# Kernel tuning notes

Measured on AMD Instinct MI355X. Metric: run time of the kernel, lower is better.

## Reference

```python
import jax, jax.numpy as jnp
import numpy as np

B_MOL = 512      # molecules in batch
A_PER = 64       # atoms per molecule (uniform -> scopes are regular)
EU_PER = 2 * A_PER   # undirected bonds per molecule (ring + skip ring)
ED_PER = 2 * EU_PER  # directed bonds per molecule
N_ATOMS = B_MOL * A_PER
N_DIR = B_MOL * ED_PER
AF, BF = 98, 111
H, HEADS, DEPTH, MLP = 256, 8, 10, 512
DK = H // HEADS
ATOM_OUT, BOND_OUT = 128, 32


def _graph_indices():
    ar = np.arange(A_PER)
    su = np.concatenate([ar, ar])
    du = np.concatenate([(ar + 1) % A_PER, (ar + 2) % A_PER])
    src = np.concatenate([su, du])   # directed: fwd then rev copies
    dst = np.concatenate([du, su])
    rev = np.concatenate([np.arange(EU_PER) + EU_PER, np.arange(EU_PER)])
    offa = (np.arange(B_MOL) * A_PER)[:, None]
    offb = (np.arange(B_MOL) * ED_PER)[:, None]
    b2a = (src[None] + offa).reshape(-1).astype(np.int32)
    b2t = (dst[None] + offa).reshape(-1).astype(np.int32)
    b2rev = (rev[None] + offb).reshape(-1).astype(np.int32)
    pairs = np.stack([(su[None] + offa).reshape(-1), (du[None] + offa).reshape(-1)], 1).astype(np.int32)
    return jnp.asarray(b2a), jnp.asarray(b2t), jnp.asarray(b2rev), jnp.asarray(pairs)


def setup_inputs() -> dict:
    key = jax.random.key(0)
    ks = jax.random.split(key, 24)
    g = lambda k, s: jax.random.normal(k, s, jnp.float32) / np.sqrt(s[0])
    b2a, b2t, b2rev, bond_pairs = _graph_indices()
    return {
        'f_atoms': jax.random.normal(ks[0], (N_ATOMS, AF), jnp.float32),
        'f_bonds': jax.random.normal(ks[1], (N_DIR, BF), jnp.float32),
        'prev_hid': jnp.zeros((N_ATOMS, H), jnp.float32),
        'b2a': b2a, 'b2t': b2t, 'b2rev': b2rev, 'bond_pairs': bond_pairs,
        'W_i': g(ks[2], (BF, H)), 'W_h': g(ks[3], (H, H)),
        'W_o': g(ks[4], (AF + H, H)), 'b_o': jnp.zeros((H,), jnp.float32),
        'Wq': g(ks[5], (H, H)), 'Wk': g(ks[6], (H, H)),
        'Wv': g(ks[7], (H, H)), 'Wattn': g(ks[8], (H, H)),
        'W_vv': jnp.eye(H, dtype=jnp.float32), 'W_vc': g(ks[9], (H, H)),
        'A1': g(ks[10], (H, MLP)), 'a1': jnp.zeros((MLP,), jnp.float32),
        'A2': g(ks[11], (MLP, ATOM_OUT)), 'a2': jnp.zeros((ATOM_OUT,), jnp.float32),
        'B1': g(ks[12], (2 * H, MLP)), 'b1': jnp.zeros((MLP,), jnp.float32),
        'B2': g(ks[13], (MLP, BOND_OUT)), 'b2b': jnp.zeros((BOND_OUT,), jnp.float32),
        'G1': g(ks[14], (H, MLP)), 'g1': jnp.zeros((MLP,), jnp.float32),
        'G2': g(ks[15], (MLP, 1)), 'g2': jnp.zeros((1,), jnp.float32),
    }


def reference(f_atoms, f_bonds, prev_hid, b2a, b2t, b2rev, bond_pairs,
              W_i, W_h, W_o, b_o, Wq, Wk, Wv, Wattn, W_vv, W_vc,
              A1, a1, A2, a2, B1, b1, B2, b2b, G1, g1, G2, g2):
    # ---- DMPNN encoder (directed bond messages) ----
    h0 = jax.nn.relu(f_bonds @ W_i)                     # [E_dir, H]
    h = h0
    for _ in range(DEPTH - 1):
        a_sum = jax.ops.segment_sum(h, b2t, num_segments=N_ATOMS)  # incoming msg per atom
        m = a_sum[b2a] - h[b2rev]                       # exclude reverse bond
        h = jax.nn.relu(h0 + m @ W_h)
    a_in = jax.ops.segment_sum(h, b2t, num_segments=N_ATOMS)
    a_feats = jax.nn.relu(jnp.concatenate([f_atoms, a_in], 1) @ W_o + b_o)  # [N, H]

    # ---- Global_Attention over per-molecule scopes (uniform sizes -> reshape) ----
    x = a_feats.reshape(B_MOL, A_PER, H)
    q = (x @ Wq).reshape(B_MOL, A_PER, HEADS, DK)
    k = (x @ Wk).reshape(B_MOL, A_PER, HEADS, DK)
    v = (x @ Wv).reshape(B_MOL, A_PER, HEADS, DK)
    scores = jnp.einsum('bqhd,bkhd->bhqk', q, k) / np.sqrt(DK)
    attn = jax.nn.softmax(scores, axis=-1)
    ctx = jnp.einsum('bhqk,bkhd->bqhd', attn, v).reshape(B_MOL, A_PER, H)
    a_feats = (x + ctx @ Wattn).reshape(N_ATOMS, H)     # residual MHA

    # ---- recurrent atom state update ----
    atom_feats = jax.nn.relu(prev_hid @ W_vv.T + a_feats @ W_vc.T)  # [N, H]

    # ---- gather-based readout heads ----
    bond_feats = jnp.concatenate([atom_feats[bond_pairs[:, 0]],
                                  atom_feats[bond_pairs[:, 1]]], axis=1)  # [E_und, 2H]
    graph_vecs = atom_feats.reshape(B_MOL, A_PER, H).sum(axis=1)          # [B, H]

    atom_outs = jax.nn.relu(atom_feats @ A1 + a1) @ A2 + a2   # [N, ATOM_OUT]
    bond_outs = jax.nn.relu(bond_feats @ B1 + b1) @ B2 + b2b  # [E_und, BOND_OUT]
    graph_outs = jax.nn.relu(graph_vecs @ G1 + g1) @ G2 + g2  # [B, 1]

    # per-molecule edit scores: [bond scores | atom scores | graph score]
    edit_scores = jnp.concatenate([bond_outs.reshape(B_MOL, -1),
                                   atom_outs.reshape(B_MOL, -1),
                                   graph_outs], axis=1)
    return edit_scores
```

## Files before the change

kernel.cpp:

```cpp
#include <hip/hip_runtime.h>
#include <cstdint>
#include <cstddef>

#define B_MOL 512
#define A_PER 64
#define ED_PER 256
#define N_ATOMS (B_MOL * A_PER)
#define N_DIR (B_MOL * ED_PER)
#define N_UND (B_MOL * 128)
#define HID 256
#define OUT_STRIDE 12289
#define AP 40
#define CP 72

typedef __attribute__((ext_vector_type(8))) short bf16x8;
typedef __attribute__((ext_vector_type(8))) unsigned short u16x8;
typedef __attribute__((ext_vector_type(4))) float f32x4;

#define MFMA(a, b, c) __builtin_amdgcn_mfma_f32_16x16x32_bf16(a, b, c, 0, 0, 0)

__device__ __forceinline__ float b2f(unsigned short s) {
  return __builtin_bit_cast(float, (unsigned)s << 16);
}
__device__ __forceinline__ void split2(float v, unsigned short& h, unsigned short& l) {
  unsigned ub = __builtin_bit_cast(unsigned, v);
  h = (unsigned short)(ub >> 16);
  float fh = __builtin_bit_cast(float, ub & 0xffff0000u);
  float r = v - fh;
  l = (unsigned short)(__builtin_bit_cast(unsigned, r) >> 16);
}
__device__ __forceinline__ unsigned short f2bf_rne(float v) {
  unsigned u = __builtin_bit_cast(unsigned, v);
  u += 0x7FFFu + ((u >> 16) & 1u);
  return (unsigned short)(u >> 16);
}
__device__ __forceinline__ int e_src(int e) {
  return (e < 64) ? e : (e < 128) ? (e - 64)
       : (e < 192) ? ((e - 127) & 63) : ((e - 190) & 63);
}

__global__ __launch_bounds__(256) void convAll(
    const float* Wi, const float* Wh, const float* Wo,
    const float* Wq, const float* Wk, const float* Wv,
    const float* Wattn, const float* Wvc, const float* Wvv,
    const float* A1, const float* A2, const float* B1, const float* B2,
    const float* fbF, unsigned short* fbT,
    unsigned short* WiTh, unsigned short* WiTl,
    unsigned short* WhTh, unsigned short* WhTl,
    unsigned short* WoTh, unsigned short* WoTl,
    unsigned short* WqkvTh, unsigned short* WqkvTl,
    unsigned short* WaTh, unsigned short* WaTl,
    unsigned short* Wcv2Th, unsigned short* Wcv2Tl,
    unsigned short* A1Th, unsigned short* A1Tl,
    unsigned short* A2Th, unsigned short* A2Tl,
    unsigned short* B1bTh, unsigned short* B1bTl,
    unsigned short* B2Th, unsigned short* B2Tl) {
  int b = blockIdx.x;
  if (b >= 3744) {
    int e = (b - 3744) * 32 + (threadIdx.x >> 3);
    int ks = (threadIdx.x & 7) * 16;
    const float* s = fbF + (size_t)e * 111;
    u16x8 o0 = {0,0,0,0,0,0,0,0}, o1 = {0,0,0,0,0,0,0,0};
#pragma unroll
    for (int z = 0; z < 8; ++z) {
      int k = ks + z;
      if (k < 111) o0[z] = f2bf_rne(s[k]);
    }
#pragma unroll
    for (int z = 0; z < 8; ++z) {
      int k = ks + 8 + z;
      if (k < 111) o1[z] = f2bf_rne(s[k]);
    }
    *(u16x8*)&fbT[(size_t)e * 128 + ks] = o0;
    *(u16x8*)&fbT[(size_t)e * 128 + ks + 8] = o1;
    return;
  }
  if (b >= 1792 && b < 2048) {
    int n = b & 255;
    for (int k = threadIdx.x; k < 768; k += 256) {
      float v;
      if (k < 256) {
        v = 0.f;
        for (int j = 0; j < 256; ++j)
          v += Wattn[(size_t)k * 256 + j] * Wvc[(size_t)n * 256 + j];
      } else if (k < 512) {
        v = Wvc[(size_t)n * 256 + (k - 256)];
      } else {
        v = Wvv[(size_t)n * 256 + (k - 512)];
      }
      unsigned short h_, l_;
      split2(v, h_, l_);
      Wcv2Th[(size_t)n * 768 + k] = h_;
      Wcv2Tl[(size_t)n * 768 + k] = l_;
    }
    return;
  }
  if (b >= 2688 && b < 3712) {
    int n = b - 2688;
    int k = threadIdx.x;
    float v = (n < 512) ? B1[(size_t)k * 512 + n]
                        : B1[(size_t)(k + 256) * 512 + (n - 512)];
    unsigned short h_, l_;
    split2(v, h_, l_);
    B1bTh[(size_t)n * 256 + k] = h_;
    B1bTl[(size_t)n * 256 + k] = l_;
    return;
  }
  const float* src = nullptr;
  unsigned short *dh = nullptr, *dl = nullptr;
  int K = 256, N = 256, Kp = 256, n = 0;
  if (b < 1792) {
    int seg = b >> 8; n = b & 255;
    switch (seg) {
      case 0: src = Wi; dh = WiTh; dl = WiTl; K = 111; Kp = 128; break;
      case 1: src = Wh; dh = WhTh; dl = WhTl; break;
      case 2: src = Wo; dh = WoTh; dl = WoTl; K = 354; Kp = 384; break;
      case 3: src = Wq; dh = WqkvTh; dl = WqkvTl; break;
      case 4: src = Wk; dh = WqkvTh + 65536; dl = WqkvTl + 65536; break;
      case 5: src = Wv; dh = WqkvTh + 131072; dl = WqkvTl + 131072; break;
      default: src = Wattn; dh = WaTh; dl = WaTl; break;
    }
    for (int k = threadIdx.x; k < Kp; k += 256) {
      float v = 0.f;
      if (b >> 8 == 2) {
        if (k < 256) v = src[(size_t)(98 + k) * 256 + n];
        else if (k < 354) v = src[(size_t)(k - 256) * 256 + n];
      } else {
        if (k < K) v = src[(size_t)k * N + n];
      }
      unsigned short h_, l_;
      split2(v, h_, l_);
      dh[(size_t)n * Kp + k] = h_;
      dl[(size_t)n * Kp + k] = l_;
    }
    return;
  }
  if (b < 2560)      { n = b - 2048; src = A1; dh = A1Th; dl = A1Tl; K = 256; N = 512; Kp = 256; }
  else if (b < 2688) { n = b - 2560; src = A2; dh = A2Th; dl = A2Tl; K = 512; N = 128; Kp = 512; }
  else               { n = b - 3712; src = B2; dh = B2Th; dl = B2Tl; K = 512; N = 32;  Kp = 512; }
  for (int k = threadIdx.x; k < Kp; k += 256) {
    float v = (k < K) ? src[(size_t)k * N + n] : 0.f;
    unsigned short h_, l_;
    split2(v, h_, l_);
    dh[(size_t)n * Kp + k] = h_;
    dl[(size_t)n * Kp + k] = l_;
  }
}

template <int AMODE>
__launch_bounds__(256, 3)
__global__ void mgemm(const void* Aa_, const void* Ab_, const void* Ac_, const void* Ad_,
                      const float* __restrict__ Af32,
                      const unsigned short* __restrict__ BTh,
                      const unsigned short* __restrict__ BTl, int ldb,
                      const unsigned short* addH, const unsigned short* addL,
                      const float* __restrict__ bias,
                      const float* __restrict__ abias,
                      void* outA, void* outB,
                      int M, int N, int K, int lda, int ldco, int outcol,
                      int relu, int outmode) {
  __shared__ unsigned short AsH[128 * AP], AsL[128 * AP];
  __shared__ unsigned short BsH[128 * AP], BsL[128 * AP];
  const int tid = threadIdx.x;
  const int lane = tid & 63;
  const int l15 = lane & 15, l4 = lane >> 4;
  const int w = tid >> 6;
  const int wr = (w >> 1) * 64, wc = (w & 1) * 64;
  const int tileM = blockIdx.x * 128, tileN = blockIdx.y * 128;
  const int srow = tid >> 1;
  const int sks = (tid & 1) * 16;

  int rem = N - tileN - wc;
  int bnMax = rem >= 64 ? 4 : (rem > 0 ? (rem >> 4) : 0);

  f32x4 zf = {0.f, 0.f, 0.f, 0.f};
  f32x4 acc[4][4];
#pragma unroll
  for (int i = 0; i < 4; ++i)
#pragma unroll
    for (int j = 0; j < 4; ++j) acc[i][j] = zf;

  const int nkb = (K + 31) >> 5;
  for (int kb = 0; kb < nkb; ++kb) {
    __syncthreads();
    const int k0 = kb * 32 + sks;
    {
      const int row = tileM + srow;
      if (AMODE == 6) {
        const unsigned short* Ah = (const unsigned short*)Aa_;
        size_t bse = (size_t)row * lda + k0;
        *(u16x8*)&AsH[srow * AP + sks]     = *(const u16x8*)&Ah[bse];
        *(u16x8*)&AsH[srow * AP + sks + 8] = *(const u16x8*)&Ah[bse + 8];
      } else if (AMODE == 1 || (AMODE == 7 && k0 < 512)) {
        const unsigned short* Ah; const unsigned short* Al;
        size_t bse;
        if (AMODE == 7) {
          Ah = (k0 < 256) ? (const unsigned short*)Aa_ : (const unsigned short*)Ac_;
          Al = (k0 < 256) ? (const unsigned short*)Ab_ : (const unsigned short*)Ad_;
          bse = (size_t)row * 256 + (k0 & 255);
        } else {
          Ah = (const unsigned short*)Aa_;
          Al = (const unsigned short*)Ab_;
          bse = (size_t)row * lda + k0;
        }
        *(u16x8*)&AsH[srow * AP + sks]     = *(const u16x8*)&Ah[bse];
        *(u16x8*)&AsH[srow * AP + sks + 8] = *(const u16x8*)&Ah[bse + 8];
        *(u16x8*)&AsL[srow * AP + sks]     = *(const u16x8*)&Al[bse];
        *(u16x8*)&AsL[srow * AP + sks + 8] = *(const u16x8*)&Al[bse + 8];
      } else if (AMODE == 5) {
        int mol = row >> 7, u = row & 127;
        int a0 = (u < 64) ? u : (u - 64);
        int a1v = (u < 64) ? ((u + 1) & 63) : ((u - 62) & 63);
        size_t p1 = (size_t)(mol * 64 + a0) * 1024 + k0;
        size_t p2 = (size_t)(mol * 64 + a1v) * 1024 + 512 + k0;
        const unsigned short* Ph = (const unsigned short*)Aa_;
        const unsigned short* Pl = (const unsigned short*)Ab_;
        u16x8 x1h[2] = {*(const u16x8*)&Ph[p1], *(const u16x8*)&Ph[p1 + 8]};
        u16x8 x1l[2] = {*(const u16x8*)&Pl[p1], *(const u16x8*)&Pl[p1 + 8]};
        u16x8 x2h[2] = {*(const u16x8*)&Ph[p2], *(const u16x8*)&Ph[p2 + 8]};
        u16x8 x2l[2] = {*(const u16x8*)&Pl[p2], *(const u16x8*)&Pl[p2 + 8]};
#pragma unroll
        for (int c = 0; c < 2; ++c) {
          u16x8 hv, lv;
#pragma unroll
          for (int z = 0; z < 8; ++z) {
            float v = b2f(x1h[c][z]) + b2f(x1l[c][z])
                    + b2f(x2h[c][z]) + b2f(x2l[c][z]) + abias[k0 + c * 8 + z];
            v = fmaxf(v, 0.f);
            unsigned short h_, l_;
            split2(v, h_, l_);
            hv[z] = h_; lv[z] = l_;
          }
          *(u16x8*)&AsH[srow * AP + sks + c * 8] = hv;
          *(u16x8*)&AsL[srow * AP + sks + c * 8] = lv;
        }
      } else if (AMODE == 8 && k0 < 256) {
        int mol = row >> 6, t = row & 63;
        const float* hb = Af32 + (size_t)mol * 65536;
        int ea0 = (t + 63) & 63;
        int ea1 = 64 + ((t + 62) & 63);
        int ea2 = 128 + t;
        int ea3 = 192 + t;
#pragma unroll
        for (int half = 0; half < 2; ++half) {
          int kk = k0 + half * 8;
          f32x4 s0, s1;
          {
            const float* p = hb + (size_t)ea0 * 256 + kk;
            s0 = *(const f32x4*)p;
            s1 = *(const f32x4*)(p + 4);
          }
          {
            const float* p = hb + (size_t)ea1 * 256 + kk;
            s0 += *(const f32x4*)p;
            s1 += *(const f32x4*)(p + 4);
          }
          {
            const float* p = hb + (size_t)ea2 * 256 + kk;
            s0 += *(const f32x4*)p;
            s1 += *(const f32x4*)(p + 4);
          }
          {
            const float* p = hb + (size_t)ea3 * 256 + kk;
            s0 += *(const f32x4*)p;
            s1 += *(const f32x4*)(p + 4);
          }
          u16x8 hv, lv;
#pragma unroll
          for (int z = 0; z < 4; ++z) {
            unsigned short h_, l_;
            split2(s0[z], h_, l_); hv[z] = h_; lv[z] = l_;
            split2(s1[z], h_, l_); hv[4 + z] = h_; lv[4 + z] = l_;
          }
          *(u16x8*)&AsH[srow * AP + sks + half * 8] = hv;
          *(u16x8*)&AsL[srow * AP + sks + half * 8] = lv;
        }
      } else {
        u16x8 hv0 = {0,0,0,0,0,0,0,0}, lv0 = {0,0,0,0,0,0,0,0};
        u16x8 hv1 = {0,0,0,0,0,0,0,0}, lv1 = {0,0,0,0,0,0,0,0};
#pragma unroll
        for (int z = 0; z < 16; ++z) {
          int k = k0 + z;
          float v = 0.f;
          if (AMODE == 0) {
            if (k < K) v = ((const float*)Aa_)[(size_t)row * lda + k];
          } else if (AMODE == 2) {
            if (k < 256) v = ((const float*)Aa_)[(size_t)row * 256 + k];
            else if (k < 354) v = ((const float*)Ab_)[(size_t)row * 98 + (k - 256)];
          } else if (AMODE == 8) {
            if (k < 354) v = ((const float*)Ab_)[(size_t)row * 98 + (k - 256)];
          } else {
            v = Af32[(size_t)row * 256 + (k - 512)];
          }
          unsigned short h_, l_;
          split2(v, h_, l_);
          if (z < 8) { hv0[z] = h_; lv0[z] = l_; }
          else       { hv1[z - 8] = h_; lv1[z - 8] = l_; }
        }
        *(u16x8*)&AsH[srow * AP + sks]     = hv0;
        *(u16x8*)&AsH[srow * AP + sks + 8] = hv1;
        *(u16x8*)&AsL[srow * AP + sks]     = lv0;
        *(u16x8*)&AsL[srow * AP + sks + 8] = lv1;
      }
    }
    {
      const int n = tileN + srow;
      if (n < N) {
        size_t bb = (size_t)n * ldb + k0;
        *(u16x8*)&BsH[srow * AP + sks]     = *(const u16x8*)&BTh[bb];
        *(u16x8*)&BsH[srow * AP + sks + 8] = *(const u16x8*)&BTh[bb + 8];
        *(u16x8*)&BsL[srow * AP + sks]     = *(const u16x8*)&BTl[bb];
        *(u16x8*)&BsL[srow * AP + sks + 8] = *(const u16x8*)&BTl[bb + 8];
      } else {
        u16x8 z8 = {0,0,0,0,0,0,0,0};
        *(u16x8*)&BsH[srow * AP + sks]     = z8;
        *(u16x8*)&BsH[srow * AP + sks + 8] = z8;
        *(u16x8*)&BsL[srow * AP + sks]     = z8;
        *(u16x8*)&BsL[srow * AP + sks + 8] = z8;
      }
    }
    __syncthreads();
    bf16x8 ah[4], al[4];
#pragma unroll
    for (int am = 0; am < 4; ++am) {
      int ar = wr + am * 16 + l15;
      ah[am] = *(const bf16x8*)&AsH[ar * AP + l4 * 8];
      if (AMODE != 6) al[am] = *(const bf16x8*)&AsL[ar * AP + l4 * 8];
    }
#pragma unroll
    for (int bn = 0; bn < 4; ++bn) {
      if (bn < bnMax) {
        int br = wc + bn * 16 + l15;
        bf16x8 bh = *(const bf16x8*)&BsH[br * AP + l4 * 8];
        bf16x8 bl = *(const bf16x8*)&BsL[br * AP + l4 * 8];
#pragma unroll
        for (int am = 0; am < 4; ++am) {
          acc[am][bn] = MFMA(ah[am], bh, acc[am][bn]);
          acc[am][bn] = MFMA(ah[am], bl, acc[am][bn]);
          if (AMODE != 6) acc[am][bn] = MFMA(al[am], bh, acc[am][bn]);
        }
      }
    }
  }

#pragma unroll
  for (int am = 0; am < 4; ++am) {
#pragma unroll
    for (int bn = 0; bn < 4; ++bn) {
      if (bn >= bnMax) continue;
      int col = tileN + wc + bn * 16 + l15;
      float bs = bias ? bias[col] : 0.f;
#pragma unroll
      for (int r = 0; r < 4; ++r) {
        size_t row = (size_t)tileM + wr + am * 16 + l4 * 4 + r;
        float v = acc[am][bn][r] + bs;
        if (addH) v += b2f(addH[row * 256 + col]) + b2f(addL[row * 256 + col]);
        if (relu) v = fmaxf(v, 0.f);
        if (outmode == 0) {
          unsigned short h_, l_;
          split2(v, h_, l_);
          ((unsigned short*)outA)[row * (size_t)ldco + col] = h_;
          ((unsigned short*)outB)[row * (size_t)ldco + col] = l_;
        } else if (outmode == 1) {
          ((float*)outA)[row * (size_t)ldco + outcol + col] = v;
        } else if (outmode == 2) {
          int mol = (int)(row >> 6), t = (int)(row & 63);
          ((float*)outA)[(size_t)mol * OUT_STRIDE + 4096 + t * 128 + col] = v;
        } else {
          int mol = (int)(row >> 7), u = (int)(row & 127);
          ((float*)outA)[(size_t)mol * OUT_STRIDE + u * 32 + col] = v;
        }
      }
    }
  }
}

__launch_bounds__(1024)
__global__ void msg_f4(float* h,
                       const unsigned short* __restrict__ WhTh,
                       const unsigned short* __restrict__ WhTl,
                       const unsigned short* __restrict__ WiTh,
                       const unsigned short* __restrict__ WiTl,
                       const unsigned short* __restrict__ fbT) {
  extern __shared__ char smem_[];
  unsigned short* AsC = (unsigned short*)smem_;
  unsigned short* BsC = (unsigned short*)(smem_ + 36864);
  const int tid = threadIdx.x;
  const int lane = tid & 63, l15 = lane & 15, l4 = lane >> 4;
  const int w = tid >> 6;
  const int wm = (w >> 2) * 64;
  const int wn = (w & 3) * 64;
  const int mol = blockIdx.x;
  const int arow = tid >> 2;
  const int aks = (tid & 3) * 8;

  f32x4 acc[4][4];
#pragma unroll
  for (int i = 0; i < 4; ++i)
#pragma unroll
    for (int j = 0; j < 4; ++j) acc[i][j] = (f32x4){0.f, 0.f, 0.f, 0.f};

  const int sA = e_src(arow);
  const int rvA = (arow < 128) ? (arow + 128) : (arow - 128);
  const int i0 = (sA + 63) & 63;
  const int i1 = 64 + ((sA + 62) & 63);
  const int i2 = 128 + sA;
  const int i3 = 192 + sA;
  const size_t hbase = (size_t)mol * 256 * 256;

  const size_t fbb = (size_t)(mol * 256 + arow) * 128;
  for (int kb = 0; kb < 4; ++kb) {
    __syncthreads();
    {
      *(u16x8*)&AsC[arow * CP + aks] = *(const u16x8*)&fbT[fbb + kb * 32 + aks];
    }
    {
      size_t bb = (size_t)arow * 128 + kb * 32 + aks;
      *(u16x8*)&BsC[arow * CP + aks]      = *(const u16x8*)&WiTh[bb];
      *(u16x8*)&BsC[arow * CP + 32 + aks] = *(const u16x8*)&WiTl[bb];
    }
    __syncthreads();
    bf16x8 ah[4];
#pragma unroll
    for (int am = 0; am < 4; ++am) {
      int ar = wm + am * 16 + l15;
      ah[am] = *(const bf16x8*)&AsC[ar * CP + l4 * 8];
    }
#pragma unroll
    for (int bn = 0; bn < 4; ++bn) {
      int br = wn + bn * 16 + l15;
      bf16x8 bh = *(const bf16x8*)&BsC[br * CP + l4 * 8];
      bf16x8 bl = *(const bf16x8*)&BsC[br * CP + 32 + l4 * 8];
#pragma unroll
      for (int am = 0; am < 4; ++am) {
        acc[am][bn] = MFMA(ah[am], bh, acc[am][bn]);
        acc[am][bn] = MFMA(ah[am], bl, acc[am][bn]);
      }
    }
  }
#pragma unroll
  for (int i = 0; i < 4; ++i)
#pragma unroll
    for (int j = 0; j < 4; ++j)
#pragma unroll
      for (int r = 0; r < 4; ++r) acc[i][j][r] = fmaxf(acc[i][j][r], 0.f);

  for (int kb = 0; kb < 8; ++kb) {
    __syncthreads();
    {
      const int c0 = kb * 32 + aks;
      f32x4 m0, m1;
      {
        const float* p = &h[hbase + (size_t)i0 * 256 + c0];
        m0 = *(const f32x4*)p;
        m1 = *(const f32x4*)(p + 4);
      }
      {
        const float* p = &h[hbase + (size_t)i1 * 256 + c0];
        m0 += *(const f32x4*)p;
        m1 += *(const f32x4*)(p + 4);
      }
      {
        const float* p = &h[hbase + (size_t)i2 * 256 + c0];
        m0 += *(const f32x4*)p;
        m1 += *(const f32x4*)(p + 4);
      }
      {
        const float* p = &h[hbase + (size_t)i3 * 256 + c0];
        m0 += *(const f32x4*)p;
        m1 += *(const f32x4*)(p + 4);
      }
      {
        const float* p = &h[hbase + (size_t)rvA * 256 + c0];
        m0 -= *(const f32x4*)p;
        m1 -= *(const f32x4*)(p + 4);
      }
      u16x8 hv, lv;
#pragma unroll
      for (int z = 0; z < 4; ++z) {
        unsigned short h_, l_;
        split2(m0[z], h_, l_); hv[z] = h_; lv[z] = l_;
        split2(m1[z], h_, l_); hv[4 + z] = h_; lv[4 + z] = l_;
      }
      *(u16x8*)&AsC[arow * CP + aks]      = hv;
      *(u16x8*)&AsC[arow * CP + 32 + aks] = lv;
    }
    {
      size_t bb = (size_t)arow * 256 + kb * 32 + aks;
      *(u16x8*)&BsC[arow * CP + aks]      = *(const u16x8*)&WhTh[bb];
      *(u16x8*)&BsC[arow * CP + 32 + aks] = *(const u16x8*)&WhTl[bb];
    }
    __syncthreads();
    bf16x8 ah[4], al[4];
#pragma unroll
    for (int am = 0; am < 4; ++am) {
      int ar = wm + am * 16 + l15;
      ah[am] = *(const bf16x8*)&AsC[ar * CP + l4 * 8];
      al[am] = *(const bf16x8*)&AsC[ar * CP + 32 + l4 * 8];
    }
#pragma unroll
    for (int bn = 0; bn < 4; ++bn) {
      int br = wn + bn * 16 + l15;
      bf16x8 bh = *(const bf16x8*)&BsC[br * CP + l4 * 8];
      bf16x8 bl = *(const bf16x8*)&BsC[br * CP + 32 + l4 * 8];
#pragma unroll
      for (int am = 0; am < 4; ++am) {
        acc[am][bn] = MFMA(ah[am], bh, acc[am][bn]);
        acc[am][bn] = MFMA(ah[am], bl, acc[am][bn]);
        acc[am][bn] = MFMA(al[am], bh, acc[am][bn]);
      }
    }
  }

#pragma unroll
  for (int am = 0; am < 4; ++am) {
#pragma unroll
    for (int r = 0; r < 4; ++r) {
      int row = wm + am * 16 + l4 * 4 + r;
      size_t rowb = hbase + (size_t)row * 256;
#pragma unroll
      for (int bn = 0; bn < 4; ++bn) {
        int col = wn + bn * 16 + l15;
        h[rowb + col] = fmaxf(acc[am][bn][r], 0.f);
      }
    }
  }
}

__global__ __launch_bounds__(64) void attn_k(const float* __restrict__ qkv,
                                             unsigned short* __restrict__ ctxH,
                                             unsigned short* __restrict__ ctxL) {
  __shared__ float kls[64 * 32];
  __shared__ float vls[64 * 32];
  int mol = blockIdx.x >> 3, head = blockIdx.x & 7;
  int lane = threadIdx.x;
  size_t rb = ((size_t)(mol * 64 + lane)) * 768 + head * 32;
#pragma unroll
  for (int c = 0; c < 8; ++c) {
    *(float4*)(kls + lane * 32 + c * 4) = *(const float4*)(qkv + rb + 256 + c * 4);
    *(float4*)(vls + lane * 32 + c * 4) = *(const float4*)(qkv + rb + 512 + c * 4);
  }
  float q[32];
#pragma unroll
  for (int d = 0; d < 32; ++d) q[d] = qkv[rb + d];
  __syncthreads();
  float mx = -1e30f, l = 0.f;
  float acc[32];
#pragma unroll
  for (int d = 0; d < 32; ++d) acc[d] = 0.f;
  for (int j = 0; j < 64; ++j) {
    float s = 0.f;
#pragma unroll
    for (int d = 0; d < 32; ++d) s += q[d] * kls[j * 32 + d];
    s *= 0.17677669529663687f;
    float nm = fmaxf(mx, s);
    float co = __expf(mx - nm);
    float p = __expf(s - nm);
    l = l * co + p;
#pragma unroll
    for (int d = 0; d < 32; ++d) acc[d] = acc[d] * co + p * vls[j * 32 + d];
    mx = nm;
  }
  float inv = 1.f / l;
  size_t ob = ((size_t)(mol * 64 + lane)) * 256 + head * 32;
#pragma unroll
  for (int d = 0; d < 32; ++d) {
    unsigned short h_, l_;
    split2(acc[d] * inv, h_, l_);
    ctxH[ob + d] = h_;
    ctxL[ob + d] = l_;
  }
}

__global__ __launch_bounds__(512) void gvh_k(const unsigned short* __restrict__ afH,
                                             const unsigned short* __restrict__ afL,
                                             const float* __restrict__ G1,
                                             const float* __restrict__ g1,
                                             const float* __restrict__ G2,
                                             const float* __restrict__ g2,
                                             float* __restrict__ out) {
  __shared__ float xs[256];
  __shared__ float red[512];
  int mol = blockIdx.x, j = threadIdx.x;
  if (j < 256) {
    float s = 0.f;
    for (int a = 0; a < 64; ++a) {
      size_t i = ((size_t)mol * 64 + a) * 256 + j;
      s += b2f(afH[i]) + b2f(afL[i]);
    }
    xs[j] = s;
  }
  __syncthreads();
  float s = 0.f;
  for (int k = 0; k < 256; ++k) s += xs[k] * G1[k * 512 + j];
  s = fmaxf(s + g1[j], 0.f);
  red[j] = s * G2[j];
  __syncthreads();
  for (int st = 256; st > 0; st >>= 1) {
    if (j < st) red[j] += red[j + st];
    __syncthreads();
  }
  if (j == 0) out[(size_t)mol * OUT_STRIDE + 12288] = red[0] + g2[0];
}

extern "C" void kernel_launch(void* const* d_in, const int* in_sizes, int n_in,
                              void* d_out, int out_size, void* d_ws, size_t ws_size,
                              hipStream_t stream) {
  (void)in_sizes; (void)n_in; (void)out_size; (void)ws_size;
  const float* f_atoms  = (const float*)d_in[0];
  const float* f_bonds  = (const float*)d_in[1];
  const float* prev_hid = (const float*)d_in[2];
  const float* W_i   = (const float*)d_in[7];
  const float* W_h   = (const float*)d_in[8];
  const float* W_o   = (const float*)d_in[9];
  const float* b_o   = (const float*)d_in[10];
  const float* Wq    = (const float*)d_in[11];
  const float* Wk    = (const float*)d_in[12];
  const float* Wv    = (const float*)d_in[13];
  const float* Wattn = (const float*)d_in[14];
  const float* W_vv  = (const float*)d_in[15];
  const float* W_vc  = (const float*)d_in[16];
  const float* A1    = (const float*)d_in[17];
  const float* a1    = (const float*)d_in[18];
  const float* A2    = (const float*)d_in[19];
  const float* a2    = (const float*)d_in[20];
  const float* B1    = (const float*)d_in[21];
  const float* b1    = (const float*)d_in[22];
  const float* B2    = (const float*)d_in[23];
  const float* b2b   = (const float*)d_in[24];
  const float* G1    = (const float*)d_in[25];
  const float* g1    = (const float*)d_in[26];
  const float* G2    = (const float*)d_in[27];
  const float* g2    = (const float*)d_in[28];
  float* out = (float*)d_out;

  char* base = (char*)d_ws;
  float* h = (float*)(base);
  unsigned short* fbT = (unsigned short*)(base + 134217728);
  char* W0 = base + 167772160;
  unsigned short* WiTh   = (unsigned short*)(W0);
  unsigned short* WiTl   = (unsigned short*)(W0 + 65536);
  unsigned short* WhTh   = (unsigned short*)(W0 + 131072);
  unsigned short* WhTl   = (unsigned short*)(W0 + 262144);
  unsigned short* WoTh   = (unsigned short*)(W0 + 393216);
  unsigned short* WoTl   = (unsigned short*)(W0 + 589824);
  unsigned short* WqkvTh = (unsigned short*)(W0 + 786432);
  unsigned short* WqkvTl = (unsigned short*)(W0 + 1179648);
  unsigned short* WaTh   = (unsigned short*)(W0 + 1572864);
  unsigned short* WaTl   = (unsigned short*)(W0 + 1703936);
  unsigned short* Wcv2Th = (unsigned short*)(W0 + 1835008);
  unsigned short* Wcv2Tl = (unsigned short*)(W0 + 2228224);
  unsigned short* A1Th   = (unsigned short*)(W0 + 2621440);
  unsigned short* A1Tl   = (unsigned short*)(W0 + 2883584);
  unsigned short* A2Th   = (unsigned short*)(W0 + 3145728);
  unsigned short* A2Tl   = (unsigned short*)(W0 + 3276800);
  unsigned short* B1bTh  = (unsigned short*)(W0 + 3407872);
  unsigned short* B1bTl  = (unsigned short*)(W0 + 3932160);
  unsigned short* B2Th   = (unsigned short*)(W0 + 4456448);
  unsigned short* B2Tl   = (unsigned short*)(W0 + 4489216);
  unsigned short* xAh  = (unsigned short*)(base + 134217728);
  unsigned short* xAl  = (unsigned short*)(base + 150994944);
  float* qkv           = (float*)(base + 33554432);
  unsigned short* ctxh = (unsigned short*)(base);
  unsigned short* ctxl = (unsigned short*)(base + 16777216);
  unsigned short* atfh = (unsigned short*)(base + 67108864);
  unsigned short* atfl = (unsigned short*)(base + 83886080);
  unsigned short* t1h  = (unsigned short*)(base);
  unsigned short* t1l  = (unsigned short*)(base + 33554432);
  unsigned short* Ph   = (unsigned short*)(base);
  unsigned short* Pl   = (unsigned short*)(base + 100663296);

  convAll<<<7840, 256, 0, stream>>>(
      W_i, W_h, W_o, Wq, Wk, Wv, Wattn, W_vc, W_vv, A1, A2, B1, B2,
      f_bonds, fbT,
      WiTh, WiTl, WhTh, WhTl, WoTh, WoTl, WqkvTh, WqkvTl, WaTh, WaTl,
      Wcv2Th, Wcv2Tl, A1Th, A1Tl, A2Th, A2Tl, B1bTh, B1bTl, B2Th, B2Tl);

  mgemm<6><<<dim3(1024, 2), 256, 0, stream>>>(
      fbT, nullptr, nullptr, nullptr, nullptr, WiTh, WiTl, 128,
      nullptr, nullptr, nullptr, nullptr,
      h, nullptr, N_DIR, 256, 128, 128, 256, 0, 1, 1);

  for (int d = 0; d < 9; ++d) {
    msg_f4<<<512, 1024, 73728, stream>>>(h, WhTh, WhTl, WiTh, WiTl, fbT);
  }

  mgemm<8><<<dim3(256, 2), 256, 0, stream>>>(
      nullptr, f_atoms, nullptr, nullptr, h, WoTh, WoTl, 384,
      nullptr, nullptr, b_o, nullptr,
      xAh, xAl, N_ATOMS, 256, 354, 0, 256, 0, 1, 0);
  mgemm<1><<<dim3(256, 6), 256, 0, stream>>>(
      xAh, xAl, nullptr, nullptr, nullptr, WqkvTh, WqkvTl, 256,
      nullptr, nullptr, nullptr, nullptr,
      qkv, nullptr, N_ATOMS, 768, 256, 256, 768, 0, 0, 1);
  attn_k<<<4096, 64, 0, stream>>>(qkv, ctxh, ctxl);
  mgemm<7><<<dim3(256, 2), 256, 0, stream>>>(
      ctxh, ctxl, xAh, xAl, prev_hid, Wcv2Th, Wcv2Tl, 768,
      nullptr, nullptr, nullptr, nullptr,
      atfh, atfl, N_ATOMS, 256, 768, 256, 256, 0, 1, 0);
  mgemm<1><<<dim3(256, 4), 256, 0, stream>>>(
      atfh, atfl, nullptr, nullptr, nullptr, A1Th, A1Tl, 256,
      nullptr, nullptr, a1, nullptr,
      t1h, t1l, N_ATOMS, 512, 256, 256, 512, 0, 1, 0);
  mgemm<1><<<dim3(256, 1), 256, 0, stream>>>(
      t1h, t1l, nullptr, nullptr, nullptr, A2Th, A2Tl, 512,
      nullptr, nullptr, a2, nullptr,
      out, nullptr, N_ATOMS, 128, 512, 512, 0, 0, 0, 2);
  mgemm<1><<<dim3(256, 8), 256, 0, stream>>>(
      atfh, atfl, nullptr, nullptr, nullptr, B1bTh, B1bTl, 256,
      nullptr, nullptr, nullptr, nullptr,
      Ph, Pl, N_ATOMS, 1024, 256, 256, 1024, 0, 0, 0);
  mgemm<5><<<dim3(512, 1), 256, 0, stream>>>(
      Ph, Pl, nullptr, nullptr, nullptr, B2Th, B2Tl, 512,
      nullptr, nullptr, b2b, b1,
      out, nullptr, N_UND, 32, 512, 0, 0, 0, 0, 3);
  gvh_k<<<512, 512, 0, stream>>>(atfh, atfl, G1, g1, G2, g2, out);
}
```

Baseline: 1.724 ms.

## Double-buffer LDS in fused message-passing kernel to overlap staging with MFMA

Turns the msg kernel's two separate K loops (the W_i input part and the W_h message part) into a single 12-chunk loop with two LDS buffers. Chunk c+1 is staged while chunk c is computed, so there is one barrier per chunk instead of two. LDS use doubles to 144KB per block. That fits the 160KB LDS on MI355X, but with 1024-thread blocks only one block fits per CU either way. The relu on the input part is applied after chunk 3. The reads of h for the next chunk now overlap with MFMA work, which may add register pressure.

```diff
diff --git a/kernel.cpp b/kernel.cpp
--- a/kernel.cpp
+++ b/kernel.cpp
@@ -12,6 +12,7 @@
 #define OUT_STRIDE 12289
 #define AP 40
 #define CP 72
+#define BUFB 73728
 
 typedef __attribute__((ext_vector_type(8))) short bf16x8;
 typedef __attribute__((ext_vector_type(8))) unsigned short u16x8;
@@ -376,15 +377,13 @@
 }
 
 __launch_bounds__(1024)
-__global__ void msg_f4(float* h,
+__global__ void msg_f6(float* h,
                        const unsigned short* __restrict__ WhTh,
                        const unsigned short* __restrict__ WhTl,
                        const unsigned short* __restrict__ WiTh,
                        const unsigned short* __restrict__ WiTl,
                        const unsigned short* __restrict__ fbT) {
   extern __shared__ char smem_[];
-  unsigned short* AsC = (unsigned short*)smem_;
-  unsigned short* BsC = (unsigned short*)(smem_ + 36864);
   const int tid = threadIdx.x;
   const int lane = tid & 63, l15 = lane & 15, l4 = lane >> 4;
   const int w = tid >> 6;
@@ -407,48 +406,18 @@
   const int i2 = 128 + sA;
   const int i3 = 192 + sA;
   const size_t hbase = (size_t)mol * 256 * 256;
-
   const size_t fbb = (size_t)(mol * 256 + arow) * 128;
-  for (int kb = 0; kb < 4; ++kb) {
-    __syncthreads();
-    {
-      *(u16x8*)&AsC[arow * CP + aks] = *(const u16x8*)&fbT[fbb + kb * 32 + aks];
-    }
-    {
-      size_t bb = (size_t)arow * 128 + kb * 32 + aks;
+
+  auto STAGE = [&](int b, int c) {
+    unsigned short* AsC = (unsigned short*)(smem_ + b * BUFB);
+    unsigned short* BsC = (unsigned short*)(smem_ + b * BUFB + 36864);
+    if (c < 4) {
+      *(u16x8*)&AsC[arow * CP + aks] = *(const u16x8*)&fbT[fbb + c * 32 + aks];
+      size_t bb = (size_t)arow * 128 + c * 32 + aks;
       *(u16x8*)&BsC[arow * CP + aks]      = *(const u16x8*)&WiTh[bb];
       *(u16x8*)&BsC[arow * CP + 32 + aks] = *(const u16x8*)&WiTl[bb];
-    }
-    __syncthreads();
-    bf16x8 ah[4];
-#pragma unroll
-    for (int am = 0; am < 4; ++am) {
-      int ar = wm + am * 16 + l15;
-      ah[am] = *(const bf16x8*)&AsC[ar * CP + l4 * 8];
-    }
-#pragma unroll
-    for (int bn = 0; bn < 4; ++bn) {
-      int br = wn + bn * 16 + l15;
-      bf16x8 bh = *(const bf16x8*)&BsC[br * CP + l4 * 8];
-      bf16x8 bl = *(const bf16x8*)&BsC[br * CP + 32 + l4 * 8];
-#pragma unroll
-      for (int am = 0; am < 4; ++am) {
-        acc[am][bn] = MFMA(ah[am], bh, acc[am][bn]);
-        acc[am][bn] = MFMA(ah[am], bl, acc[am][bn]);
-      }
-    }
-  }
-#pragma unroll
-  for (int i = 0; i < 4; ++i)
-#pragma unroll
-    for (int j = 0; j < 4; ++j)
-#pragma unroll
-      for (int r = 0; r < 4; ++r) acc[i][j][r] = fmaxf(acc[i][j][r], 0.f);
-
-  for (int kb = 0; kb < 8; ++kb) {
-    __syncthreads();
-    {
-      const int c0 = kb * 32 + aks;
+    } else {
+      const int c0 = (c - 4) * 32 + aks;
       f32x4 m0, m1;
       {
         const float* p = &h[hbase + (size_t)i0 * 256 + c0];
@@ -484,31 +453,68 @@
       }
       *(u16x8*)&AsC[arow * CP + aks]      = hv;
       *(u16x8*)&AsC[arow * CP + 32 + aks] = lv;
-    }
-    {
-      size_t bb = (size_t)arow * 256 + kb * 32 + aks;
+      size_t bb = (size_t)arow * 256 + (c - 4) * 32 + aks;
       *(u16x8*)&BsC[arow * CP + aks]      = *(const u16x8*)&WhTh[bb];
       *(u16x8*)&BsC[arow * CP + 32 + aks] = *(const u16x8*)&WhTl[bb];
     }
+  };
+
+  auto COMPUTE = [&](int b, int c) {
+    unsigned short* AsC = (unsigned short*)(smem_ + b * BUFB);
+    unsigned short* BsC = (unsigned short*)(smem_ + b * BUFB + 36864);
+    if (c < 4) {
+      bf16x8 ah[4];
+#pragma unroll
+      for (int am = 0; am < 4; ++am) {
+        int ar = wm + am * 16 + l15;
+        ah[am] = *(const bf16x8*)&AsC[ar * CP + l4 * 8];
+      }
+#pragma unroll
+      for (int bn = 0; bn < 4; ++bn) {
+        int br = wn + bn * 16 + l15;
+        bf16x8 bh = *(const bf16x8*)&BsC[br * CP + l4 * 8];
+        bf16x8 bl = *(const bf16x8*)&BsC[br * CP + 32 + l4 * 8];
+#pragma unroll
+        for (int am = 0; am < 4; ++am) {
+          acc[am][bn] = MFMA(ah[am], bh, acc[am][bn]);
+          acc[am][bn] = MFMA(ah[am], bl, acc[am][bn]);
+        }
+      }
+    } else {
+      bf16x8 ah[4], al[4];
+#pragma unroll
+      for (int am = 0; am < 4; ++am) {
+        int ar = wm + am * 16 + l15;
+        ah[am] = *(const bf16x8*)&AsC[ar * CP + l4 * 8];
+        al[am] = *(const bf16x8*)&AsC[ar * CP + 32 + l4 * 8];
+      }
+#pragma unroll
+      for (int bn = 0; bn < 4; ++bn) {
+        int br = wn + bn * 16 + l15;
+        bf16x8 bh = *(const bf16x8*)&BsC[br * CP + l4 * 8];
+        bf16x8 bl = *(const bf16x8*)&BsC[br * CP + 32 + l4 * 8];
+#pragma unroll
+        for (int am = 0; am < 4; ++am) {
+          acc[am][bn] = MFMA(ah[am], bh, acc[am][bn]);
+          acc[am][bn] = MFMA(ah[am], bl, acc[am][bn]);
+          acc[am][bn] = MFMA(al[am], bh, acc[am][bn]);
+        }
+      }
+    }
+  };
+
+  STAGE(0, 0);
+  for (int c = 0; c < 12; ++c) {
     __syncthreads();
-    bf16x8 ah[4], al[4];
-#pragma unroll
-    for (int am = 0; am < 4; ++am) {
-      int ar = wm + am * 16 + l15;
-      ah[am] = *(const bf16x8*)&AsC[ar * CP + l4 * 8];
-      al[am] = *(const bf16x8*)&AsC[ar * CP + 32 + l4 * 8];
-    }
-#pragma unroll
-    for (int bn = 0; bn < 4; ++bn) {
-      int br = wn + bn * 16 + l15;
-      bf16x8 bh = *(const bf16x8*)&BsC[br * CP + l4 * 8];
-      bf16x8 bl = *(const bf16x8*)&BsC[br * CP + 32 + l4 * 8];
-#pragma unroll
-      for (int am = 0; am < 4; ++am) {
-        acc[am][bn] = MFMA(ah[am], bh, acc[am][bn]);
-        acc[am][bn] = MFMA(ah[am], bl, acc[am][bn]);
-        acc[am][bn] = MFMA(al[am], bh, acc[am][bn]);
-      }
+    if (c + 1 < 12) STAGE((c + 1) & 1, c + 1);
+    COMPUTE(c & 1, c);
+    if (c == 3) {
+#pragma unroll
+      for (int i = 0; i < 4; ++i)
+#pragma unroll
+        for (int j = 0; j < 4; ++j)
+#pragma unroll
+          for (int r = 0; r < 4; ++r) acc[i][j][r] = fmaxf(acc[i][j][r], 0.f);
     }
   }
 
@@ -682,7 +688,7 @@
       h, nullptr, N_DIR, 256, 128, 128, 256, 0, 1, 1);
 
   for (int d = 0; d < 9; ++d) {
-    msg_f4<<<512, 1024, 73728, stream>>>(h, WhTh, WhTl, WiTh, WiTl, fbT);
+    msg_f6<<<512, 1024, 2 * BUFB, stream>>>(h, WhTh, WhTl, WiTh, WiTl, fbT);
   }
 
   mgemm<8><<<dim3(256, 2), 256, 0, stream>>>(
```

New measurement: 1.617 ms. 6.2% less time.
